# Kernel optimization log

Hardware: AMD Instinct MI355X
Metric: run time of the kernel (lower is better)

The kernel has to match this reference:

```python
import jax, jax.numpy as jnp
import numpy as np

S = 1.05  # fixed scale constant from the module


def setup_inputs() -> dict:
    key = jax.random.key(0)
    k1, k2 = jax.random.split(key)
    N, C = 32768, 2048
    source_output = jax.random.normal(k1, (N, C), dtype=jnp.float32)
    source_label = jax.random.randint(k2, (N,), 0, C, dtype=jnp.int64)
    return {"source_output": source_output, "source_label": source_label}


def reference(source_output, source_label):
    N, C = source_output.shape
    lbl = source_label.astype(jnp.int32)

    # Per-class (group) std over ALL elements of the group's [n_j, C] logit block,
    # biased (unbiased=False), detached (stop_gradient), times 0.5.
    row_sum = jnp.sum(source_output, axis=1)            # [N]
    row_sq = jnp.sum(source_output * source_output, 1)  # [N]
    g_sum = jax.ops.segment_sum(row_sum, lbl, num_segments=C)   # [C]
    g_sq = jax.ops.segment_sum(row_sq, lbl, num_segments=C)     # [C]
    g_cnt = jax.ops.segment_sum(jnp.ones((N,), source_output.dtype), lbl,
                                num_segments=C) * C              # elements per group
    cnt = jnp.maximum(g_cnt, 1.0)
    mean = g_sum / cnt
    var = jnp.maximum(g_sq / cnt - mean * mean, 0.0)
    m = jax.lax.stop_gradient(jnp.sqrt(var) * 0.5)               # [C]
    m_row = m[lbl]                                               # [N]

    # Margin-adjust only the target-class logit of each row.
    logit_c = jnp.take_along_axis(source_output, lbl[:, None], axis=1)[:, 0]  # [N]
    val = jnp.where(logit_c > 0, (logit_c - m_row) / S, (logit_c - m_row) * S)

    is_tgt = lbl[:, None] == jnp.arange(C, dtype=jnp.int32)[None, :]          # [N,C]
    new_logits = jnp.where(is_tgt, val[:, None], source_output)

    # nll_loss(log_softmax) = mean cross-entropy at target index (row order
    # from grouping is irrelevant for the mean).
    logp = jax.nn.log_softmax(new_logits, axis=-1)
    nll = -jnp.take_along_axis(logp, lbl[:, None], axis=1)[:, 0]
    return jnp.mean(nll)
```

## Files before the change

kernel.cpp:

```cpp
#include <hip/hip_runtime.h>
#include <math.h>

#define N_ROWS 32768
#define N_COLS 2048
constexpr float S_CONST = 1.05f;

__device__ __forceinline__ float wave_reduce_sum(float v) {
    #pragma unroll
    for (int off = 32; off > 0; off >>= 1) v += __shfl_down(v, off, 64);
    return v;
}
__device__ __forceinline__ float wave_reduce_max(float v) {
    #pragma unroll
    for (int off = 32; off > 0; off >>= 1) v = fmaxf(v, __shfl_down(v, off, 64));
    return v;
}

__global__ __launch_bounds__(256) void k_rowpass(
    const float* __restrict__ X, const long long* __restrict__ lbl,
    float* __restrict__ g_sum, float* __restrict__ g_sq, float* __restrict__ g_cnt,
    float* __restrict__ row_max, float* __restrict__ row_se, float* __restrict__ row_lc)
{
    const int row  = blockIdx.x;
    const int t    = threadIdx.x;
    const int wave = t >> 6;
    const int lane = t & 63;
    const int col  = (int)lbl[row];

    const float4* xr = (const float4*)(X + (size_t)row * N_COLS);
    float4 v0 = xr[t];
    float4 v1 = xr[t + 256];
    float vals[8] = {v0.x, v0.y, v0.z, v0.w, v1.x, v1.y, v1.z, v1.w};

    __shared__ float s_lc;
    __shared__ float sh[12];
    __shared__ float s_bmax, s_bsum, s_bsq;

    float sum = 0.f, sq = 0.f;
    #pragma unroll
    for (int i = 0; i < 8; i++) {
        int j = (i < 4) ? (t * 4 + i) : ((t + 256) * 4 + (i - 4));
        float x = vals[i];
        sum += x;
        sq = fmaf(x, x, sq);
        if (j == col) { s_lc = x; vals[i] = -INFINITY; }
    }
    float mx = -INFINITY;
    #pragma unroll
    for (int i = 0; i < 8; i++) mx = fmaxf(mx, vals[i]);

    float wsum = wave_reduce_sum(sum);
    float wsq  = wave_reduce_sum(sq);
    float wmx  = wave_reduce_max(mx);
    if (lane == 0) { sh[wave] = wsum; sh[4 + wave] = wsq; sh[8 + wave] = wmx; }
    __syncthreads();
    if (t == 0) {
        s_bsum = sh[0] + sh[1] + sh[2] + sh[3];
        s_bsq  = sh[4] + sh[5] + sh[6] + sh[7];
        s_bmax = fmaxf(fmaxf(sh[8], sh[9]), fmaxf(sh[10], sh[11]));
    }
    __syncthreads();

    const float bmax = s_bmax;
    float se = 0.f;
    #pragma unroll
    for (int i = 0; i < 8; i++) se += expf(vals[i] - bmax);

    float wse = wave_reduce_sum(se);
    if (lane == 0) sh[wave] = wse;
    __syncthreads();
    if (t == 0) {
        float bse = sh[0] + sh[1] + sh[2] + sh[3];
        row_max[row] = bmax;
        row_se[row]  = bse;
        row_lc[row]  = s_lc;
        atomicAdd(&g_sum[col], s_bsum);
        atomicAdd(&g_sq[col],  s_bsq);
        atomicAdd(&g_cnt[col], 1.0f);
    }
}

__global__ __launch_bounds__(256) void k_classm(
    const float* __restrict__ g_sum, const float* __restrict__ g_sq,
    const float* __restrict__ g_cnt, float* __restrict__ m)
{
    int c = blockIdx.x * 256 + threadIdx.x;
    if (c >= N_COLS) return;
    float cnt  = fmaxf(g_cnt[c] * (float)N_COLS, 1.0f);
    float mean = g_sum[c] / cnt;
    float var  = fmaxf(g_sq[c] / cnt - mean * mean, 0.0f);
    m[c] = 0.5f * sqrtf(var);
}

__global__ __launch_bounds__(256) void k_nll(
    const long long* __restrict__ lbl, const float* __restrict__ m,
    const float* __restrict__ row_max, const float* __restrict__ row_se,
    const float* __restrict__ row_lc, float* __restrict__ out)
{
    float acc = 0.f;
    for (int n = blockIdx.x * blockDim.x + threadIdx.x; n < N_ROWS;
         n += gridDim.x * blockDim.x) {
        int   c   = (int)lbl[n];
        float x   = row_lc[n];
        float mm  = m[c];
        float xm  = x - mm;
        float val = (x > 0.f) ? (xm / S_CONST) : (xm * S_CONST);
        float rmx = row_max[n];
        float M   = fmaxf(rmx, val);
        float lse = logf(row_se[n] * expf(rmx - M) + expf(val - M)) + M;
        acc += (lse - val);
    }
    __shared__ float sh[4];
    float w = wave_reduce_sum(acc);
    int wave = threadIdx.x >> 6, lane = threadIdx.x & 63;
    if (lane == 0) sh[wave] = w;
    __syncthreads();
    if (threadIdx.x == 0) {
        float b = sh[0] + sh[1] + sh[2] + sh[3];
        atomicAdd(out, b * (1.0f / (float)N_ROWS));
    }
}

extern "C" void kernel_launch(void* const* d_in, const int* in_sizes, int n_in,
                              void* d_out, int out_size, void* d_ws, size_t ws_size,
                              hipStream_t stream) {
    const float*     X   = (const float*)d_in[0];
    const long long* lbl = (const long long*)d_in[1];
    float*           out = (float*)d_out;
    float*           ws  = (float*)d_ws;

    const int C = N_COLS, N = N_ROWS;
    float* g_sum   = ws;
    float* g_sq    = ws + C;
    float* g_cnt   = ws + 2 * C;
    float* m       = ws + 3 * C;
    float* row_max = ws + 4 * C;
    float* row_se  = row_max + N;
    float* row_lc  = row_se + N;

    hipMemsetAsync(ws, 0, 3 * C * sizeof(float), stream);
    hipMemsetAsync(d_out, 0, sizeof(float), stream);

    k_rowpass<<<N, 256, 0, stream>>>(X, lbl, g_sum, g_sq, g_cnt, row_max, row_se, row_lc);
    k_classm<<<(C + 255) / 256, 256, 0, stream>>>(g_sum, g_sq, g_cnt, m);
    k_nll<<<64, 256, 0, stream>>>(lbl, m, row_max, row_se, row_lc, out);
}
```

Measured before the change: 360.8 us.

## Map one row per wavefront and fold class-margin computation into NLL kernel

The row pass now assigns one wavefront per row with four rows per block, so reductions use only xor-shuffles and need no shared memory or block barriers. The per-class margin kernel is removed and its arithmetic is recomputed inside the NLL kernel, and the two memsets become a single init kernel. Fast __expf replaces expf in the row sum-of-exponentials. This cuts launches and synchronisation in exchange for 32 loads per lane and slightly lower exp precision.

Result: no change. 359.6 us (-0.4%).

```diff
diff --git a/kernel.cpp b/kernel.cpp
--- a/kernel.cpp
+++ b/kernel.cpp
@@ -5,15 +5,22 @@
 #define N_COLS 2048
 constexpr float S_CONST = 1.05f;
 
-__device__ __forceinline__ float wave_reduce_sum(float v) {
+__device__ __forceinline__ float wred_sum(float v) {
     #pragma unroll
-    for (int off = 32; off > 0; off >>= 1) v += __shfl_down(v, off, 64);
+    for (int off = 32; off > 0; off >>= 1) v += __shfl_xor(v, off, 64);
     return v;
 }
-__device__ __forceinline__ float wave_reduce_max(float v) {
+__device__ __forceinline__ float wred_max(float v) {
     #pragma unroll
-    for (int off = 32; off > 0; off >>= 1) v = fmaxf(v, __shfl_down(v, off, 64));
+    for (int off = 32; off > 0; off >>= 1) v = fmaxf(v, __shfl_xor(v, off, 64));
     return v;
+}
+
+__global__ __launch_bounds__(256) void k_init(float* __restrict__ ws,
+                                              float* __restrict__ out) {
+    int i = blockIdx.x * 256 + threadIdx.x;
+    if (i < 3 * N_COLS) ws[i] = 0.f;
+    if (i == 0) out[0] = 0.f;
 }
 
 __global__ __launch_bounds__(256) void k_rowpass(
@@ -21,97 +28,80 @@
     float* __restrict__ g_sum, float* __restrict__ g_sq, float* __restrict__ g_cnt,
     float* __restrict__ row_max, float* __restrict__ row_se, float* __restrict__ row_lc)
 {
-    const int row  = blockIdx.x;
-    const int t    = threadIdx.x;
-    const int wave = t >> 6;
-    const int lane = t & 63;
+    const int lane = threadIdx.x & 63;
+    const int row  = blockIdx.x * 4 + (threadIdx.x >> 6);
     const int col  = (int)lbl[row];
 
     const float4* xr = (const float4*)(X + (size_t)row * N_COLS);
-    float4 v0 = xr[t];
-    float4 v1 = xr[t + 256];
-    float vals[8] = {v0.x, v0.y, v0.z, v0.w, v1.x, v1.y, v1.z, v1.w};
+    float4 v[8];
+    #pragma unroll
+    for (int k = 0; k < 8; k++) v[k] = xr[lane + 64 * k];
 
-    __shared__ float s_lc;
-    __shared__ float sh[12];
-    __shared__ float s_bmax, s_bsum, s_bsq;
+    float sum = 0.f, sq = 0.f, mx = -INFINITY, lc = 0.f;
+    #pragma unroll
+    for (int k = 0; k < 8; k++) {
+        const int base = 4 * (lane + 64 * k);
+        float e0 = v[k].x, e1 = v[k].y, e2 = v[k].z, e3 = v[k].w;
+        sum += e0 + e1 + e2 + e3;
+        sq = fmaf(e0, e0, sq); sq = fmaf(e1, e1, sq);
+        sq = fmaf(e2, e2, sq); sq = fmaf(e3, e3, sq);
+        if (base + 0 == col) { lc = e0; e0 = -INFINITY; }
+        if (base + 1 == col) { lc = e1; e1 = -INFINITY; }
+        if (base + 2 == col) { lc = e2; e2 = -INFINITY; }
+        if (base + 3 == col) { lc = e3; e3 = -INFINITY; }
+        mx = fmaxf(fmaxf(mx, fmaxf(e0, e1)), fmaxf(e2, e3));
+        v[k].x = e0; v[k].y = e1; v[k].z = e2; v[k].w = e3;
+    }
+    sum = wred_sum(sum);
+    sq  = wred_sum(sq);
+    mx  = wred_max(mx);
+    lc  = __shfl(lc, (col >> 2) & 63, 64);
 
-    float sum = 0.f, sq = 0.f;
-    #pragma unroll
-    for (int i = 0; i < 8; i++) {
-        int j = (i < 4) ? (t * 4 + i) : ((t + 256) * 4 + (i - 4));
-        float x = vals[i];
-        sum += x;
-        sq = fmaf(x, x, sq);
-        if (j == col) { s_lc = x; vals[i] = -INFINITY; }
-    }
-    float mx = -INFINITY;
-    #pragma unroll
-    for (int i = 0; i < 8; i++) mx = fmaxf(mx, vals[i]);
-
-    float wsum = wave_reduce_sum(sum);
-    float wsq  = wave_reduce_sum(sq);
-    float wmx  = wave_reduce_max(mx);
-    if (lane == 0) { sh[wave] = wsum; sh[4 + wave] = wsq; sh[8 + wave] = wmx; }
-    __syncthreads();
-    if (t == 0) {
-        s_bsum = sh[0] + sh[1] + sh[2] + sh[3];
-        s_bsq  = sh[4] + sh[5] + sh[6] + sh[7];
-        s_bmax = fmaxf(fmaxf(sh[8], sh[9]), fmaxf(sh[10], sh[11]));
-    }
-    __syncthreads();
-
-    const float bmax = s_bmax;
     float se = 0.f;
     #pragma unroll
-    for (int i = 0; i < 8; i++) se += expf(vals[i] - bmax);
+    for (int k = 0; k < 8; k++) {
+        se += __expf(v[k].x - mx);
+        se += __expf(v[k].y - mx);
+        se += __expf(v[k].z - mx);
+        se += __expf(v[k].w - mx);
+    }
+    se = wred_sum(se);
 
-    float wse = wave_reduce_sum(se);
-    if (lane == 0) sh[wave] = wse;
-    __syncthreads();
-    if (t == 0) {
-        float bse = sh[0] + sh[1] + sh[2] + sh[3];
-        row_max[row] = bmax;
-        row_se[row]  = bse;
-        row_lc[row]  = s_lc;
-        atomicAdd(&g_sum[col], s_bsum);
-        atomicAdd(&g_sq[col],  s_bsq);
+    if (lane == 0) {
+        row_max[row] = mx;
+        row_se[row]  = se;
+        row_lc[row]  = lc;
+        atomicAdd(&g_sum[col], sum);
+        atomicAdd(&g_sq[col],  sq);
         atomicAdd(&g_cnt[col], 1.0f);
     }
 }
 
-__global__ __launch_bounds__(256) void k_classm(
+__global__ __launch_bounds__(256) void k_nll(
+    const long long* __restrict__ lbl,
     const float* __restrict__ g_sum, const float* __restrict__ g_sq,
-    const float* __restrict__ g_cnt, float* __restrict__ m)
-{
-    int c = blockIdx.x * 256 + threadIdx.x;
-    if (c >= N_COLS) return;
-    float cnt  = fmaxf(g_cnt[c] * (float)N_COLS, 1.0f);
-    float mean = g_sum[c] / cnt;
-    float var  = fmaxf(g_sq[c] / cnt - mean * mean, 0.0f);
-    m[c] = 0.5f * sqrtf(var);
-}
-
-__global__ __launch_bounds__(256) void k_nll(
-    const long long* __restrict__ lbl, const float* __restrict__ m,
+    const float* __restrict__ g_cnt,
     const float* __restrict__ row_max, const float* __restrict__ row_se,
     const float* __restrict__ row_lc, float* __restrict__ out)
 {
     float acc = 0.f;
     for (int n = blockIdx.x * blockDim.x + threadIdx.x; n < N_ROWS;
          n += gridDim.x * blockDim.x) {
-        int   c   = (int)lbl[n];
-        float x   = row_lc[n];
-        float mm  = m[c];
-        float xm  = x - mm;
-        float val = (x > 0.f) ? (xm / S_CONST) : (xm * S_CONST);
-        float rmx = row_max[n];
-        float M   = fmaxf(rmx, val);
-        float lse = logf(row_se[n] * expf(rmx - M) + expf(val - M)) + M;
+        int   c    = (int)lbl[n];
+        float cnt  = fmaxf(g_cnt[c] * (float)N_COLS, 1.0f);
+        float mean = g_sum[c] / cnt;
+        float var  = fmaxf(g_sq[c] / cnt - mean * mean, 0.0f);
+        float mm   = 0.5f * sqrtf(var);
+        float x    = row_lc[n];
+        float xm   = x - mm;
+        float val  = (x > 0.f) ? (xm / S_CONST) : (xm * S_CONST);
+        float rmx  = row_max[n];
+        float M    = fmaxf(rmx, val);
+        float lse  = logf(row_se[n] * expf(rmx - M) + expf(val - M)) + M;
         acc += (lse - val);
     }
     __shared__ float sh[4];
-    float w = wave_reduce_sum(acc);
+    float w = wred_sum(acc);
     int wave = threadIdx.x >> 6, lane = threadIdx.x & 63;
     if (lane == 0) sh[wave] = w;
     __syncthreads();
@@ -133,15 +123,13 @@
     float* g_sum   = ws;
     float* g_sq    = ws + C;
     float* g_cnt   = ws + 2 * C;
-    float* m       = ws + 3 * C;
-    float* row_max = ws + 4 * C;
+    float* row_max = ws + 3 * C;
     float* row_se  = row_max + N;
     float* row_lc  = row_se + N;
 
-    hipMemsetAsync(ws, 0, 3 * C * sizeof(float), stream);
-    hipMemsetAsync(d_out, 0, sizeof(float), stream);
-
-    k_rowpass<<<N, 256, 0, stream>>>(X, lbl, g_sum, g_sq, g_cnt, row_max, row_se, row_lc);
-    k_classm<<<(C + 255) / 256, 256, 0, stream>>>(g_sum, g_sq, g_cnt, m);
-    k_nll<<<64, 256, 0, stream>>>(lbl, m, row_max, row_se, row_lc, out);
+    k_init<<<(3 * C + 255) / 256, 256, 0, stream>>>(ws, out);
+    k_rowpass<<<N / 4, 256, 0, stream>>>(X, lbl, g_sum, g_sq, g_cnt,
+                                         row_max, row_se, row_lc);
+    k_nll<<<64, 256, 0, stream>>>(lbl, g_sum, g_sq, g_cnt,
+                                  row_max, row_se, row_lc, out);
 }
```
